# Kernel tuning notes

Measured on AMD Instinct MI355X. Metric: run time of the kernel, lower is better.

Reference implementation:

```python
import jax, jax.numpy as jnp
import numpy as np
import math

PHI = (1.0 + math.sqrt(5.0)) / 2.0
TWO_PI = 2.0 * math.pi
LUT_SIZE = 4096  # matches get_global_lut(4096, device)

_LUT_SIN = jnp.sin(jnp.arange(LUT_SIZE, dtype=jnp.float32) * (TWO_PI / LUT_SIZE))
_LUT_COS = jnp.cos(jnp.arange(LUT_SIZE, dtype=jnp.float32) * (TWO_PI / LUT_SIZE))


def lut_sin_cos(theta):
    """Linearly-interpolated sin/cos lookup over a 4096-entry table on [0, 2pi)."""
    pos = jnp.mod(theta, TWO_PI) * (LUT_SIZE / TWO_PI)
    i0f = jnp.floor(pos)
    frac = pos - i0f
    i0 = i0f.astype(jnp.int32) % LUT_SIZE
    i1 = (i0 + 1) % LUT_SIZE
    sin_v = _LUT_SIN[i0] * (1.0 - frac) + _LUT_SIN[i1] * frac
    cos_v = _LUT_COS[i0] * (1.0 - frac) + _LUT_COS[i1] * frac
    return sin_v, cos_v


def setup_inputs() -> dict:
    key = jax.random.key(0)
    ks = jax.random.split(key, 6)
    B, D = 8192, 2048
    return {
        "x_real": jax.random.normal(ks[0], (B, D), dtype=jnp.float32),
        "x_imag": jax.random.normal(ks[1], (B, D), dtype=jnp.float32),
        "t": jax.random.uniform(ks[2], (B,), dtype=jnp.float32) * 100.0,
        "w_query": jax.random.normal(ks[3], (D,), dtype=jnp.float32) * 0.02,
        "b_query": jnp.zeros((D,), dtype=jnp.float32),
        "w_osc": jax.random.normal(ks[4], (D,), dtype=jnp.float32) * 0.02,
        "b_osc": jnp.zeros((D,), dtype=jnp.float32),
        "memory_real": jnp.zeros((B, D), dtype=jnp.float32),
        "memory_imag": jnp.zeros((B, D), dtype=jnp.float32),
    }


def reference(x_real, x_imag, t, w_query, b_query, w_osc, b_osc,
              memory_real, memory_imag):
    d_model = x_real.shape[-1]
    scale = math.sqrt(d_model)
    k = 1.0  # default sensitivity

    t_phi = t[:, None] * PHI  # [B, 1]

    # Query phase via LUT
    wl_query = 1.0 + jnp.abs(w_query)
    theta_query = x_real / wl_query + b_query
    sin_q, cos_q = lut_sin_cos(theta_query)  # query_imag, query_real

    # complex_full interference
    interf_real = jnp.sum(cos_q * x_real + sin_q * x_imag, axis=-1)  # [B]
    interf_imag = jnp.sum(cos_q * x_imag - sin_q * x_real, axis=-1)  # [B]
    interference = jnp.sqrt(interf_real ** 2 + interf_imag ** 2)
    interference_norm = jax.nn.sigmoid(interference / scale - 2.0)
    x_inv = 1.0 - interference_norm
    alpha = jnp.exp(-k * x_inv)[:, None]  # [B, 1]

    # Exponential memory blend (memory is detached / constant)
    blended_real = alpha * x_real + (1.0 - alpha) * memory_real
    blended_imag = alpha * x_imag + (1.0 - alpha) * memory_imag

    # Oscillator evolution via second LUT pass
    wl_osc = 1.0 + jnp.abs(w_osc)
    theta_osc_real = blended_real / wl_osc + b_osc + t_phi
    theta_osc_imag = blended_imag / wl_osc + b_osc + t_phi
    sin_or, cos_or = lut_sin_cos(theta_osc_real)
    sin_oi, cos_oi = lut_sin_cos(theta_osc_imag)
    evolved_real = cos_or * cos_oi - sin_or * sin_oi
    evolved_imag = cos_or * sin_oi + sin_or * cos_oi
    return evolved_real, evolved_imag
```

## Files before the change

kernel.cpp:

```cpp
#include <hip/hip_runtime.h>
#include <math.h>


#define PHI_F 1.61803398874989f

__device__ __forceinline__ void k1_step(
    const float4* __restrict__ xr4, const float4* __restrict__ xi4,
    const float4* __restrict__ wq4, const float4* __restrict__ bq4,
    int c, float& aR, float& aI)
{
    float4 xr = xr4[c];
    float4 xi = xi4[c];
    float4 wq = wq4[c];
    float4 bq = bq4[c];
    #pragma unroll
    for (int j = 0; j < 4; ++j) {
        float xrv = (&xr.x)[j];
        float xiv = (&xi.x)[j];
        float wl  = 1.f + fabsf((&wq.x)[j]);
        float th  = xrv * __builtin_amdgcn_rcpf(wl) + (&bq.x)[j];
        float sq, cq;
        __sincosf(th, &sq, &cq);
        aR = fmaf(cq, xrv, fmaf(sq, xiv, aR));
        aI = fmaf(cq, xiv, fmaf(-sq, xrv, aI));
    }
}

__global__ __launch_bounds__(256) void alpha_kernel(
    const float* __restrict__ x_real, const float* __restrict__ x_imag,
    const float* __restrict__ w_query, const float* __restrict__ b_query,
    float* __restrict__ alpha_out,
    int d4, int B, float inv_scale)
{
    const int wave = (int)threadIdx.x >> 6;
    const int lane = (int)threadIdx.x & 63;
    const int row  = ((int)blockIdx.x << 2) + wave;
    if (row >= B) return;

    const size_t base4 = (size_t)row * d4;
    const float4* xr4 = (const float4*)x_real + base4;
    const float4* xi4 = (const float4*)x_imag + base4;
    const float4* wq4 = (const float4*)w_query;
    const float4* bq4 = (const float4*)b_query;

    float aR0 = 0.f, aI0 = 0.f;
    float aR1 = 0.f, aI1 = 0.f;

    if (d4 == 512) {
        #pragma unroll
        for (int s = 0; s < 8; ++s) {
            if (s & 1) k1_step(xr4, xi4, wq4, bq4, (s << 6) + lane, aR1, aI1);
            else       k1_step(xr4, xi4, wq4, bq4, (s << 6) + lane, aR0, aI0);
        }
    } else {
        for (int c = lane; c < d4; c += 64)
            k1_step(xr4, xi4, wq4, bq4, c, aR0, aI0);
    }

    float accR = aR0 + aR1;
    float accI = aI0 + aI1;

    #pragma unroll
    for (int off = 32; off > 0; off >>= 1) {
        accR += __shfl_xor(accR, off);
        accI += __shfl_xor(accI, off);
    }

    if (lane == 0) {
        float interf = sqrtf(fmaf(accR, accR, accI * accI));
        float z      = fmaf(interf, inv_scale, -2.0f);
        float sig    = 1.f / (1.f + __expf(-z));
        alpha_out[row] = __expf(sig - 1.f);
    }
}

__global__ __launch_bounds__(256) void evolve_kernel(
    const float* __restrict__ x_real, const float* __restrict__ x_imag,
    const float* __restrict__ t_arr,
    const float* __restrict__ w_osc, const float* __restrict__ b_osc,
    const float* __restrict__ mem_r, const float* __restrict__ mem_i,
    const float* __restrict__ alpha_in,
    float* __restrict__ out_r, float* __restrict__ out_i,
    int d4)
{
    const int row = blockIdx.x;
    const float alpha = alpha_in[row];
    const float beta  = 1.f - alpha;
    const float tphi2 = 2.0f * PHI_F * t_arr[row];

    const size_t base4 = (size_t)row * d4;
    const float4* xr4 = (const float4*)x_real + base4;
    const float4* xi4 = (const float4*)x_imag + base4;
    const float4* mr4 = (const float4*)mem_r + base4;
    const float4* mi4 = (const float4*)mem_i + base4;
    const float4* wo4 = (const float4*)w_osc;
    const float4* bo4 = (const float4*)b_osc;
    float4* or4 = (float4*)out_r + base4;
    float4* oi4 = (float4*)out_i + base4;

    for (int c = (int)threadIdx.x; c < d4; c += 256) {
        float4 xr = xr4[c];
        float4 xi = xi4[c];
        float4 mr = mr4[c];
        float4 mi = mi4[c];
        float4 wo = wo4[c];
        float4 bo = bo4[c];
        float4 oR, oI;
        #pragma unroll
        for (int j = 0; j < 4; ++j) {
            float br = fmaf(alpha, (&xr.x)[j], beta * (&mr.x)[j]);
            float bi = fmaf(alpha, (&xi.x)[j], beta * (&mi.x)[j]);
            float wl = 1.f + fabsf((&wo.x)[j]);
            float ang = fmaf(br + bi, __builtin_amdgcn_rcpf(wl),
                             fmaf(2.f, (&bo.x)[j], tphi2));
            float sv, cv;
            __sincosf(ang, &sv, &cv);
            (&oR.x)[j] = cv;
            (&oI.x)[j] = sv;
        }
        or4[c] = oR;
        oi4[c] = oI;
    }
}

extern "C" void kernel_launch(void* const* d_in, const int* in_sizes, int n_in,
                              void* d_out, int out_size, void* d_ws, size_t ws_size,
                              hipStream_t stream) {
    const float* x_real   = (const float*)d_in[0];
    const float* x_imag   = (const float*)d_in[1];
    const float* t_arr    = (const float*)d_in[2];
    const float* w_query  = (const float*)d_in[3];
    const float* b_query  = (const float*)d_in[4];
    const float* w_osc    = (const float*)d_in[5];
    const float* b_osc    = (const float*)d_in[6];
    const float* mem_r    = (const float*)d_in[7];
    const float* mem_i    = (const float*)d_in[8];

    const int B = in_sizes[2];
    const int D = in_sizes[3];
    const int d4 = D >> 2;

    float* out_r = (float*)d_out;
    float* out_i = out_r + (size_t)B * D;
    float* alpha_ws = (float*)d_ws;

    const float inv_scale = 1.0f / sqrtf((float)D);

    const int grid1 = (B + 3) >> 2;
    alpha_kernel<<<grid1, 256, 0, stream>>>(
        x_real, x_imag, w_query, b_query, alpha_ws, d4, B, inv_scale);

    evolve_kernel<<<B, 256, 0, stream>>>(
        x_real, x_imag, t_arr, w_osc, b_osc, mem_r, mem_i, alpha_ws,
        out_r, out_i, d4);
}
```

Measured before the change: 338.4 us.

## Software-pipeline row loads in alpha kernel and grid-stride prefetch in evolve kernel

The alpha kernel now has each wave process four rows, double-buffering the next row's x_real/x_imag in registers while computing the current row. The evolve kernel becomes a persistent grid-stride loop over float4 elements that loads the next element's inputs before computing and storing the current one. Both changes aim to hide memory latency in these bandwidth-bound kernels. The cost is much higher register pressure, which may lower occupancy. A generic fallback path is kept for other shapes.

```diff
diff --git a/kernel.cpp b/kernel.cpp
--- a/kernel.cpp
+++ b/kernel.cpp
@@ -4,33 +4,90 @@
 
 #define PHI_F 1.61803398874989f
 
-__device__ __forceinline__ void k1_step(
+
+__device__ __forceinline__ void k1_load_row(
     const float4* __restrict__ xr4, const float4* __restrict__ xi4,
+    int lane, float4* xr, float4* xi)
+{
+    #pragma unroll
+    for (int s = 0; s < 8; ++s) {
+        int c = (s << 6) + lane;
+        xr[s] = xr4[c];
+        xi[s] = xi4[c];
+    }
+}
+
+__device__ __forceinline__ float k1_compute_row(
     const float4* __restrict__ wq4, const float4* __restrict__ bq4,
-    int c, float& aR, float& aI)
-{
-    float4 xr = xr4[c];
-    float4 xi = xi4[c];
-    float4 wq = wq4[c];
-    float4 bq = bq4[c];
-    #pragma unroll
-    for (int j = 0; j < 4; ++j) {
-        float xrv = (&xr.x)[j];
-        float xiv = (&xi.x)[j];
-        float wl  = 1.f + fabsf((&wq.x)[j]);
-        float th  = xrv * __builtin_amdgcn_rcpf(wl) + (&bq.x)[j];
-        float sq, cq;
-        __sincosf(th, &sq, &cq);
-        aR = fmaf(cq, xrv, fmaf(sq, xiv, aR));
-        aI = fmaf(cq, xiv, fmaf(-sq, xrv, aI));
-    }
-}
-
-__global__ __launch_bounds__(256) void alpha_kernel(
+    int lane, const float4* xr, const float4* xi, float inv_scale)
+{
+    float aR0 = 0.f, aI0 = 0.f, aR1 = 0.f, aI1 = 0.f;
+    #pragma unroll
+    for (int s = 0; s < 8; ++s) {
+        int c = (s << 6) + lane;
+        float4 wq = wq4[c];
+        float4 bq = bq4[c];
+        #pragma unroll
+        for (int j = 0; j < 4; ++j) {
+            float xrv = (&xr[s].x)[j];
+            float xiv = (&xi[s].x)[j];
+            float wl  = 1.f + fabsf((&wq.x)[j]);
+            float th  = xrv * __builtin_amdgcn_rcpf(wl) + (&bq.x)[j];
+            float sq, cq;
+            __sincosf(th, &sq, &cq);
+            if (s & 1) { aR1 = fmaf(cq, xrv, fmaf(sq, xiv, aR1));
+                         aI1 = fmaf(cq, xiv, fmaf(-sq, xrv, aI1)); }
+            else       { aR0 = fmaf(cq, xrv, fmaf(sq, xiv, aR0));
+                         aI0 = fmaf(cq, xiv, fmaf(-sq, xrv, aI0)); }
+        }
+    }
+    float accR = aR0 + aR1;
+    float accI = aI0 + aI1;
+    #pragma unroll
+    for (int off = 32; off > 0; off >>= 1) {
+        accR += __shfl_xor(accR, off);
+        accI += __shfl_xor(accI, off);
+    }
+    float interf = sqrtf(fmaf(accR, accR, accI * accI));
+    float z   = fmaf(interf, inv_scale, -2.0f);
+    float sig = 1.f / (1.f + __expf(-z));
+    return __expf(sig - 1.f);
+}
+
+__global__ __launch_bounds__(256) void alpha_kernel_fast(
     const float* __restrict__ x_real, const float* __restrict__ x_imag,
     const float* __restrict__ w_query, const float* __restrict__ b_query,
-    float* __restrict__ alpha_out,
-    int d4, int B, float inv_scale)
+    float* __restrict__ alpha_out, float inv_scale)
+{
+    const int wave = (int)threadIdx.x >> 6;
+    const int lane = (int)threadIdx.x & 63;
+    const int row0 = (((int)blockIdx.x << 2) + wave) << 2;
+
+    const float4* wq4 = (const float4*)w_query;
+    const float4* bq4 = (const float4*)b_query;
+    const float4* xr4 = (const float4*)x_real + ((size_t)row0 << 9);
+    const float4* xi4 = (const float4*)x_imag + ((size_t)row0 << 9);
+
+    float4 AR[8], AI[8], BR[8], BI[8];
+
+    k1_load_row(xr4,        xi4,        lane, AR, AI);
+    k1_load_row(xr4 + 512,  xi4 + 512,  lane, BR, BI);
+    float a0 = k1_compute_row(wq4, bq4, lane, AR, AI, inv_scale);
+    if (lane == 0) alpha_out[row0 + 0] = a0;
+    k1_load_row(xr4 + 1024, xi4 + 1024, lane, AR, AI);
+    float a1 = k1_compute_row(wq4, bq4, lane, BR, BI, inv_scale);
+    if (lane == 0) alpha_out[row0 + 1] = a1;
+    k1_load_row(xr4 + 1536, xi4 + 1536, lane, BR, BI);
+    float a2 = k1_compute_row(wq4, bq4, lane, AR, AI, inv_scale);
+    if (lane == 0) alpha_out[row0 + 2] = a2;
+    float a3 = k1_compute_row(wq4, bq4, lane, BR, BI, inv_scale);
+    if (lane == 0) alpha_out[row0 + 3] = a3;
+}
+
+__global__ __launch_bounds__(256) void alpha_kernel_gen(
+    const float* __restrict__ x_real, const float* __restrict__ x_imag,
+    const float* __restrict__ w_query, const float* __restrict__ b_query,
+    float* __restrict__ alpha_out, int d4, int B, float inv_scale)
 {
     const int wave = (int)threadIdx.x >> 6;
     const int lane = (int)threadIdx.x & 63;
@@ -43,45 +100,130 @@
     const float4* wq4 = (const float4*)w_query;
     const float4* bq4 = (const float4*)b_query;
 
-    float aR0 = 0.f, aI0 = 0.f;
-    float aR1 = 0.f, aI1 = 0.f;
-
-    if (d4 == 512) {
+    float aR = 0.f, aI = 0.f;
+    for (int c = lane; c < d4; c += 64) {
+        float4 xr = xr4[c];
+        float4 xi = xi4[c];
+        float4 wq = wq4[c];
+        float4 bq = bq4[c];
         #pragma unroll
-        for (int s = 0; s < 8; ++s) {
-            if (s & 1) k1_step(xr4, xi4, wq4, bq4, (s << 6) + lane, aR1, aI1);
-            else       k1_step(xr4, xi4, wq4, bq4, (s << 6) + lane, aR0, aI0);
+        for (int j = 0; j < 4; ++j) {
+            float xrv = (&xr.x)[j];
+            float xiv = (&xi.x)[j];
+            float wl  = 1.f + fabsf((&wq.x)[j]);
+            float th  = xrv * __builtin_amdgcn_rcpf(wl) + (&bq.x)[j];
+            float sq, cq;
+            __sincosf(th, &sq, &cq);
+            aR = fmaf(cq, xrv, fmaf(sq, xiv, aR));
+            aI = fmaf(cq, xiv, fmaf(-sq, xrv, aI));
         }
-    } else {
-        for (int c = lane; c < d4; c += 64)
-            k1_step(xr4, xi4, wq4, bq4, c, aR0, aI0);
-    }
-
-    float accR = aR0 + aR1;
-    float accI = aI0 + aI1;
-
+    }
     #pragma unroll
     for (int off = 32; off > 0; off >>= 1) {
-        accR += __shfl_xor(accR, off);
-        accI += __shfl_xor(accI, off);
-    }
-
+        aR += __shfl_xor(aR, off);
+        aI += __shfl_xor(aI, off);
+    }
     if (lane == 0) {
-        float interf = sqrtf(fmaf(accR, accR, accI * accI));
-        float z      = fmaf(interf, inv_scale, -2.0f);
-        float sig    = 1.f / (1.f + __expf(-z));
+        float interf = sqrtf(fmaf(aR, aR, aI * aI));
+        float z   = fmaf(interf, inv_scale, -2.0f);
+        float sig = 1.f / (1.f + __expf(-z));
         alpha_out[row] = __expf(sig - 1.f);
     }
 }
 
-__global__ __launch_bounds__(256) void evolve_kernel(
+
+struct K2Stage {
+    float4 xr, xi, mr, mi, wo, bo;
+    float  al, tp;
+};
+
+__device__ __forceinline__ K2Stage k2_load(
+    int idx,
+    const float4* __restrict__ xr4, const float4* __restrict__ xi4,
+    const float4* __restrict__ mr4, const float4* __restrict__ mi4,
+    const float4* __restrict__ wo4, const float4* __restrict__ bo4,
+    const float* __restrict__ alpha_in, const float* __restrict__ t_arr)
+{
+    K2Stage s;
+    const int row = idx >> 9;
+    const int col = idx & 511;
+    s.xr = xr4[idx];
+    s.xi = xi4[idx];
+    s.mr = mr4[idx];
+    s.mi = mi4[idx];
+    s.wo = wo4[col];
+    s.bo = bo4[col];
+    s.al = alpha_in[row];
+    s.tp = t_arr[row];
+    return s;
+}
+
+__device__ __forceinline__ void k2_compute(
+    int idx, const K2Stage& s,
+    float4* __restrict__ or4, float4* __restrict__ oi4)
+{
+    const float alpha = s.al;
+    const float beta  = 1.f - alpha;
+    const float tphi2 = 2.0f * PHI_F * s.tp;
+    float4 oR, oI;
+    #pragma unroll
+    for (int j = 0; j < 4; ++j) {
+        float br = fmaf(alpha, (&s.xr.x)[j], beta * (&s.mr.x)[j]);
+        float bi = fmaf(alpha, (&s.xi.x)[j], beta * (&s.mi.x)[j]);
+        float wl = 1.f + fabsf((&s.wo.x)[j]);
+        float ang = fmaf(br + bi, __builtin_amdgcn_rcpf(wl),
+                         fmaf(2.f, (&s.bo.x)[j], tphi2));
+        float sv, cv;
+        __sincosf(ang, &sv, &cv);
+        (&oR.x)[j] = cv;
+        (&oI.x)[j] = sv;
+    }
+    or4[idx] = oR;
+    oi4[idx] = oI;
+}
+
+__global__ __launch_bounds__(256) void evolve_kernel_fast(
     const float* __restrict__ x_real, const float* __restrict__ x_imag,
     const float* __restrict__ t_arr,
     const float* __restrict__ w_osc, const float* __restrict__ b_osc,
     const float* __restrict__ mem_r, const float* __restrict__ mem_i,
     const float* __restrict__ alpha_in,
-    float* __restrict__ out_r, float* __restrict__ out_i,
-    int d4)
+    float* __restrict__ out_r, float* __restrict__ out_i, int n4)
+{
+    const float4* xr4 = (const float4*)x_real;
+    const float4* xi4 = (const float4*)x_imag;
+    const float4* mr4 = (const float4*)mem_r;
+    const float4* mi4 = (const float4*)mem_i;
+    const float4* wo4 = (const float4*)w_osc;
+    const float4* bo4 = (const float4*)b_osc;
+    float4* or4 = (float4*)out_r;
+    float4* oi4 = (float4*)out_i;
+
+    const int stride = (int)gridDim.x << 8;
+    int i = ((int)blockIdx.x << 8) + (int)threadIdx.x;
+    if (i >= n4) return;
+
+    K2Stage A = k2_load(i, xr4, xi4, mr4, mi4, wo4, bo4, alpha_in, t_arr);
+    int j = i + stride;
+    while (j < n4) {
+        K2Stage Bs = k2_load(j, xr4, xi4, mr4, mi4, wo4, bo4, alpha_in, t_arr);
+        k2_compute(i, A, or4, oi4);
+        i = j + stride;
+        if (i >= n4) { k2_compute(j, Bs, or4, oi4); return; }
+        A = k2_load(i, xr4, xi4, mr4, mi4, wo4, bo4, alpha_in, t_arr);
+        k2_compute(j, Bs, or4, oi4);
+        j = i + stride;
+    }
+    k2_compute(i, A, or4, oi4);
+}
+
+__global__ __launch_bounds__(256) void evolve_kernel_gen(
+    const float* __restrict__ x_real, const float* __restrict__ x_imag,
+    const float* __restrict__ t_arr,
+    const float* __restrict__ w_osc, const float* __restrict__ b_osc,
+    const float* __restrict__ mem_r, const float* __restrict__ mem_i,
+    const float* __restrict__ alpha_in,
+    float* __restrict__ out_r, float* __restrict__ out_i, int d4)
 {
     const int row = blockIdx.x;
     const float alpha = alpha_in[row];
@@ -139,6 +281,7 @@
     const int B = in_sizes[2];
     const int D = in_sizes[3];
     const int d4 = D >> 2;
+    const int n4 = B * d4;
 
     float* out_r = (float*)d_out;
     float* out_i = out_r + (size_t)B * D;
@@ -146,11 +289,21 @@
 
     const float inv_scale = 1.0f / sqrtf((float)D);
 
-    const int grid1 = (B + 3) >> 2;
-    alpha_kernel<<<grid1, 256, 0, stream>>>(
-        x_real, x_imag, w_query, b_query, alpha_ws, d4, B, inv_scale);
-
-    evolve_kernel<<<B, 256, 0, stream>>>(
-        x_real, x_imag, t_arr, w_osc, b_osc, mem_r, mem_i, alpha_ws,
-        out_r, out_i, d4);
-}
+    if (d4 == 512 && (B & 15) == 0) {
+        alpha_kernel_fast<<<B >> 4, 256, 0, stream>>>(
+            x_real, x_imag, w_query, b_query, alpha_ws, inv_scale);
+
+        int grid2 = 2048;
+        if (grid2 * 256 > n4) grid2 = (n4 + 255) >> 8;
+        evolve_kernel_fast<<<grid2, 256, 0, stream>>>(
+            x_real, x_imag, t_arr, w_osc, b_osc, mem_r, mem_i, alpha_ws,
+            out_r, out_i, n4);
+    } else {
+        const int grid1 = (B + 3) >> 2;
+        alpha_kernel_gen<<<grid1, 256, 0, stream>>>(
+            x_real, x_imag, w_query, b_query, alpha_ws, d4, B, inv_scale);
+        evolve_kernel_gen<<<B, 256, 0, stream>>>(
+            x_real, x_imag, t_arr, w_osc, b_osc, mem_r, mem_i, alpha_ws,
+            out_r, out_i, d4);
+    }
+}
```

Measured after the change: 339.1 us. About the same (+0.2%).
